# Kernel tuning notes

Hardware: AMD Instinct MI355X
Metric: run time of the kernel (lower is better)

The kernel has to match this reference:

```python
import jax, jax.numpy as jnp
import numpy as np

N_NODES = 100000
N_EDGES = 1600000
EMBED_DIM = 64
NUM_HEADS = 4
HEAD_DIM = EMBED_DIM // NUM_HEADS  # 16


def mish(x):
    return x * jnp.tanh(jax.nn.softplus(x))


def setup_inputs() -> dict:
    key = jax.random.key(0)
    ks = jax.random.split(key, 8)
    x = jax.random.normal(ks[0], (N_NODES, EMBED_DIM), dtype=jnp.float32)
    senders = jax.random.randint(ks[1], (N_EDGES,), 0, N_NODES, dtype=jnp.int32)
    receivers = jax.random.randint(ks[2], (N_EDGES,), 0, N_NODES, dtype=jnp.int32)
    sc = 1.0 / np.sqrt(EMBED_DIM)
    # DenseGeneral(features=(H, d)) for senders / receivers, with bias
    Ws = jax.random.normal(ks[3], (EMBED_DIM, NUM_HEADS, HEAD_DIM), dtype=jnp.float32) * sc
    bs = jnp.zeros((NUM_HEADS, HEAD_DIM), dtype=jnp.float32)
    Wr = jax.random.normal(ks[4], (EMBED_DIM, NUM_HEADS, HEAD_DIM), dtype=jnp.float32) * sc
    br = jnp.zeros((NUM_HEADS, HEAD_DIM), dtype=jnp.float32)
    # Dense(1) on last axis (head_dim), weights shared across heads
    aw = jax.random.normal(ks[5], (HEAD_DIM,), dtype=jnp.float32) * (1.0 / np.sqrt(HEAD_DIM))
    ab = jnp.zeros((1,), dtype=jnp.float32)
    return {"x": x, "Ws": Ws, "bs": bs, "Wr": Wr, "br": br,
            "aw": aw, "ab": ab, "senders": senders, "receivers": receivers}


def reference(x, Ws, bs, Wr, br, aw, ab, senders, receivers):
    n = x.shape[0]
    # Node-level projections (same math as per-edge DenseGeneral, less traffic)
    s_proj = jnp.einsum('nf,fhd->nhd', x, Ws) + bs  # [N,H,d]
    r_proj = jnp.einsum('nf,fhd->nhd', x, Wr) + br  # [N,H,d]
    se = s_proj[senders]      # [E,H,d] gather of sender features
    re = r_proj[receivers]    # [E,H,d] gather of receiver features
    # GATv2 logit: Dense(1)(mish(s + r)) -> [E,H]
    logits = jnp.einsum('ehd,d->eh', mish(se + re), aw) + ab[0]
    # Segment softmax over incoming edges of each receiver node
    lmax = jax.ops.segment_max(logits, receivers, num_segments=n)
    ex = jnp.exp(logits - lmax[receivers])
    denom = jax.ops.segment_sum(ex, receivers, num_segments=n)
    alpha = ex / denom[receivers]  # [E,H]
    # Scatter-sum weighted sender features back to receiver nodes
    out = jax.ops.segment_sum(alpha[..., None] * se, receivers, num_segments=n)  # [N,H,d]
    return out.reshape(n, -1)  # [N, H*d]
```

## Files before the change

### kernel.cpp

```cpp
#include <hip/hip_runtime.h>
#include <hip/hip_fp16.h>
#include <math.h>

#define N_NODES 100000
#define N_EDGES 1600000
#define EMBED 64
#define HEADS 4
#define HDIM 16

#define SLOTS 64

#define BKT_SHIFT 8
#define BKT_NODES 256
#define NBKT 391
#define BKT_CAP 5120
#define TILE 4096
#define NTILE 391
#define NGRP (N_EDGES / 4)

#define NODES_BLK 64
#define NBLK_PROJ 1563
#define SMEM_BYTES 52224

#define LOG2E 1.44269504f

__device__ __forceinline__ float mish_aw(float z, float awc) {
    float ex  = __expf(fminf(z, 30.f));
    float u   = 1.f + ex;
    float den = fmaf(u, u, 1.f);
    float f   = fmaf(-2.f, __builtin_amdgcn_rcpf(den), 1.f);
    return z * awc * f;
}

template<int CTRL>
__device__ __forceinline__ float ror_add(float t) {
    int x = __builtin_amdgcn_mov_dpp(__float_as_int(t), CTRL, 0xF, 0xF, true);
    return t + __int_as_float(x);
}
__device__ __forceinline__ float head_reduce(float t) {
    t = ror_add<0x121>(t);
    t = ror_add<0x122>(t);
    t = ror_add<0x124>(t);
    t = ror_add<0x128>(t);
    return t;
}

template<int CTRL>
__device__ __forceinline__ __half2 hror_add(__half2 t) {
    int x = __builtin_amdgcn_mov_dpp(__builtin_bit_cast(int, t), CTRL, 0xF, 0xF, true);
    return __hadd2(t, __builtin_bit_cast(__half2, x));
}
__device__ __forceinline__ __half2 head_reduce_h2(__half2 t) {
    t = hror_add<0x121>(t);
    t = hror_add<0x122>(t);
    t = hror_add<0x124>(t);
    t = hror_add<0x128>(t);
    return t;
}

__global__ __launch_bounds__(256) void proj_bucketa_kernel(
        const float* __restrict__ x,
        const float* __restrict__ Ws, const float* __restrict__ bs,
        const float* __restrict__ Wr, const float* __restrict__ br,
        const int* __restrict__ senders, const int* __restrict__ receivers,
        unsigned short* __restrict__ sph, unsigned short* __restrict__ rph,
        int* __restrict__ bktcnt, int* __restrict__ bkt) {
    __shared__ __align__(16) char smem[SMEM_BYTES];
    int tid = threadIdx.x;
    if (blockIdx.x < NBLK_PROJ) {
        float* wsT = (float*)smem;
        float* wrT = wsT + 64 * 68;
        float* xsh = wrT + 64 * 68;
        for (int i = tid; i < 4096; i += 256) {
            int k = i >> 6, o = i & 63;
            wsT[o * 68 + k] = Ws[i];
            wrT[o * 68 + k] = Wr[i];
        }
        int nb = blockIdx.x * NODES_BLK;
        for (int i = 0; i < 4; ++i) {
            int g = i * 256 + tid;
            int nl = g >> 4;
            int k4 = g & 15;
            if (nb + nl < N_NODES) {
                float4 v = ((const float4*)(x + ((size_t)(nb + nl) << 6)))[k4];
                *(float4*)(xsh + nl * 68 + (k4 << 2)) = v;
            }
        }
        __syncthreads();
        int o = tid & 63;
        int w = tid >> 6;
        float bsv = bs[o], brv = br[o];
        float accs[16], accr[16];
#pragma unroll
        for (int p = 0; p < 16; ++p) { accs[p] = bsv; accr[p] = brv; }
        const float4* ws4 = (const float4*)wsT + o * 17;
        const float4* wr4 = (const float4*)wrT + o * 17;
        const float4* xs4 = (const float4*)xsh + (w << 4) * 17;
#pragma unroll 4
        for (int k4 = 0; k4 < 16; ++k4) {
            float4 a = ws4[k4];
            float4 b = wr4[k4];
#pragma unroll
            for (int p = 0; p < 16; ++p) {
                float4 xv = xs4[p * 17 + k4];
                accs[p] += xv.x * a.x + xv.y * a.y + xv.z * a.z + xv.w * a.w;
                accr[p] += xv.x * b.x + xv.y * b.y + xv.z * b.z + xv.w * b.w;
            }
        }
        int node0 = nb + (w << 4);
#pragma unroll
        for (int p = 0; p < 16; ++p) {
            int node = node0 + p;
            if (node < N_NODES) {
                sph[(node << 6) + o] = __half_as_ushort(__float2half_rn(accs[p]));
                rph[(node << 6) + o] = __half_as_ushort(__float2half_rn(accr[p]));
            }
        }
    } else {
        int* hist = (int*)smem;
        int* base = hist + NBKT;
        int* cur  = base + NBKT;
        for (int i = tid; i < NBKT; i += 256) hist[i] = 0;
        __syncthreads();
        int g0 = (blockIdx.x - NBLK_PROJ) * (TILE / 4);
        int4 r[4], s[4];
        bool v[4];
#pragma unroll
        for (int t = 0; t < 4; ++t) {
            int g = g0 + t * 256 + tid;
            v[t] = (g < NGRP);
            if (v[t]) {
                r[t] = ((const int4*)receivers)[g];
                s[t] = ((const int4*)senders)[g];
                atomicAdd(&hist[r[t].x >> BKT_SHIFT], 1);
                atomicAdd(&hist[r[t].y >> BKT_SHIFT], 1);
                atomicAdd(&hist[r[t].z >> BKT_SHIFT], 1);
                atomicAdd(&hist[r[t].w >> BKT_SHIFT], 1);
            }
        }
        __syncthreads();
        for (int i = tid; i < NBKT; i += 256) {
            int h = hist[i];
            base[i] = (h > 0) ? atomicAdd(&bktcnt[i], h) : 0;
            cur[i] = 0;
        }
        __syncthreads();
#pragma unroll
        for (int t = 0; t < 4; ++t) {
            if (v[t]) {
                int b, rk, slot;
                b = r[t].x >> BKT_SHIFT; rk = atomicAdd(&cur[b], 1); slot = base[b] + rk;
                if (slot < BKT_CAP) bkt[b * BKT_CAP + slot] = ((r[t].x & (BKT_NODES - 1)) << 17) | s[t].x;
                b = r[t].y >> BKT_SHIFT; rk = atomicAdd(&cur[b], 1); slot = base[b] + rk;
                if (slot < BKT_CAP) bkt[b * BKT_CAP + slot] = ((r[t].y & (BKT_NODES - 1)) << 17) | s[t].y;
                b = r[t].z >> BKT_SHIFT; rk = atomicAdd(&cur[b], 1); slot = base[b] + rk;
                if (slot < BKT_CAP) bkt[b * BKT_CAP + slot] = ((r[t].z & (BKT_NODES - 1)) << 17) | s[t].z;
                b = r[t].w >> BKT_SHIFT; rk = atomicAdd(&cur[b], 1); slot = base[b] + rk;
                if (slot < BKT_CAP) bkt[b * BKT_CAP + slot] = ((r[t].w & (BKT_NODES - 1)) << 17) | s[t].w;
            }
        }
    }
}

__global__ __launch_bounds__(1024) void bucketb_kernel(
        const int* __restrict__ bktcnt, const int* __restrict__ bkt,
        int* __restrict__ cursor, int* __restrict__ csr) {
    __shared__ int lcur[BKT_NODES];
    int tid = threadIdx.x;
    int b = blockIdx.x;
    if (tid < BKT_NODES) lcur[tid] = 0;
    __syncthreads();
    int cnt = bktcnt[b];
    if (cnt > BKT_CAP) cnt = BKT_CAP;
    const int* bb = bkt + b * BKT_CAP;
    for (int i = tid; i < cnt; i += 1024) {
        int vv = bb[i];
        int rl = vv >> 17;
        int sv = vv & 0x1FFFF;
        int slot = atomicAdd(&lcur[rl], 1);
        if (slot < SLOTS) csr[((((b << BKT_SHIFT) + rl)) << 6) + slot] = sv << 7;
    }
    __syncthreads();
    if (tid < BKT_NODES) {
        int node = (b << BKT_SHIFT) + tid;
        if (node < N_NODES) cursor[node] = lcur[tid];
    }
}

__global__ __launch_bounds__(256) void fused_gather_kernel(
                                    const unsigned short* __restrict__ sph,
                                    const unsigned short* __restrict__ rph,
                                    const int* __restrict__ csr,
                                    const int* __restrict__ cursor,
                                    const float* __restrict__ aw,
                                    const float* __restrict__ ab,
                                    float* __restrict__ out) {
    int wave = (blockIdx.x * blockDim.x + threadIdx.x) >> 6;
    wave = __builtin_amdgcn_readfirstlane(wave);
    int lane = threadIdx.x & 63;
    int deg = cursor[wave];
    deg = (deg > SLOTS) ? SLOTS : deg;
    const int* cbase = csr + (wave << 6);
    const char* splb = (const char*)sph + (lane << 1);
    float rp  = __half2float(__ushort_as_half(rph[(wave << 6) + lane]));
    float awc = aw[lane & 15];
    __half2 k_pk   = __float2half2_rn(LOG2E);
    __half2 rpk_pk = __float2half2_rn(rp * LOG2E);
    __half2 aw2_pk = __float2half2_rn(awc * LOG2E);
    __half2 rpa_pk = __float2half2_rn(rp * awc * LOG2E);
    __half2 ones   = __float2half2_rn(1.0f);
    __half2 neg2   = __float2half2_rn(-2.0f);
    __half2 l2   = __float2half2_rn(0.0f);
    __half2 acc2 = __float2half2_rn(0.0f);
    float l_t = 0.f, acc_t = 0.f;
    int i = 0;
    for (; i + 8 <= deg; i += 8) {
        unsigned short su[8];
#pragma unroll
        for (int j = 0; j < 8; ++j) su[j] = *(const unsigned short*)(splb + cbase[i + j]);
#pragma unroll
        for (int j = 0; j < 4; ++j) {
            __half2 sp  = __halves2half2(__ushort_as_half(su[2 * j]),
                                         __ushort_as_half(su[2 * j + 1]));
            __half2 w   = h2exp2(__hfma2(sp, k_pk, rpk_pk));
            __half2 u   = __hadd2(w, ones);
            __half2 den = __hfma2(u, u, ones);
            __half2 r   = h2rcp(den);
            __half2 f   = __hfma2(neg2, r, ones);
            __half2 za  = __hfma2(sp, aw2_pk, rpa_pk);
            __half2 tt  = head_reduce_h2(__hmul2(za, f));
            __half2 p   = h2exp2(tt);
            l2   = __hadd2(l2, p);
            acc2 = __hfma2(p, sp, acc2);
        }
    }
    for (; i + 2 <= deg; i += 2) {
        __half2 sp  = __halves2half2(__ushort_as_half(*(const unsigned short*)(splb + cbase[i])),
                                     __ushort_as_half(*(const unsigned short*)(splb + cbase[i + 1])));
        __half2 w   = h2exp2(__hfma2(sp, k_pk, rpk_pk));
        __half2 u   = __hadd2(w, ones);
        __half2 den = __hfma2(u, u, ones);
        __half2 r   = h2rcp(den);
        __half2 f   = __hfma2(neg2, r, ones);
        __half2 za  = __hfma2(sp, aw2_pk, rpa_pk);
        __half2 tt  = head_reduce_h2(__hmul2(za, f));
        __half2 p   = h2exp2(tt);
        l2   = __hadd2(l2, p);
        acc2 = __hfma2(p, sp, acc2);
    }
    if (i < deg) {
        float sp0 = __half2float(__ushort_as_half(*(const unsigned short*)(splb + cbase[i])));
        float t0 = head_reduce(mish_aw(sp0 + rp, awc));
        float p = __builtin_amdgcn_exp2f(t0 * LOG2E);
        l_t += p;
        acc_t = fmaf(p, sp0, acc_t);
    }
    float l   = __low2float(l2) + __high2float(l2) + l_t;
    float acc = __low2float(acc2) + __high2float(acc2) + acc_t;
    out[(wave << 6) + lane] = (deg > 0) ? acc * __builtin_amdgcn_rcpf(l) : 0.f;
}

extern "C" void kernel_launch(void* const* d_in, const int* in_sizes, int n_in,
                              void* d_out, int out_size, void* d_ws, size_t ws_size,
                              hipStream_t stream) {
    const float* x  = (const float*)d_in[0];
    const float* Ws = (const float*)d_in[1];
    const float* bs = (const float*)d_in[2];
    const float* Wr = (const float*)d_in[3];
    const float* br = (const float*)d_in[4];
    const float* aw = (const float*)d_in[5];
    const float* ab = (const float*)d_in[6];
    const int* senders   = (const int*)d_in[7];
    const int* receivers = (const int*)d_in[8];
    float* out = (float*)d_out;

    char* wsp = (char*)d_ws;
    unsigned short* sph = (unsigned short*)wsp;  wsp += (size_t)N_NODES * EMBED * 2;
    unsigned short* rph = (unsigned short*)wsp;  wsp += (size_t)N_NODES * EMBED * 2;
    int* csr    = (int*)wsp;  wsp += (size_t)N_NODES * SLOTS * 4;
    int* cursor = (int*)wsp;  wsp += (size_t)N_NODES * 4;
    int* bkt    = (int*)wsp;  wsp += (size_t)NBKT * BKT_CAP * 4;
    int* bktcnt = (int*)wsp;  wsp += 512 * 4;

    hipMemsetAsync(bktcnt, 0, NBKT * 4, stream);

    proj_bucketa_kernel<<<NBLK_PROJ + NTILE, 256, 0, stream>>>(
        x, Ws, bs, Wr, br, senders, receivers, sph, rph, bktcnt, bkt);

    bucketb_kernel<<<NBKT, 1024, 0, stream>>>(bktcnt, bkt, cursor, csr);

    int gather_blocks = (N_NODES * 64 + 255) / 256;
    fused_gather_kernel<<<gather_blocks, 256, 0, stream>>>(sph, rph, csr, cursor,
                                                           aw, ab, out);
}
```

Baseline: 125.6 us.

## Reorder bucketing blocks first, halve tile size, prefetch gathers with split accumulators

After: 148.7 us. 1.18x slower.

```diff
diff --git a/kernel.cpp b/kernel.cpp
--- a/kernel.cpp
+++ b/kernel.cpp
@@ -14,8 +14,8 @@
 #define BKT_NODES 256
 #define NBKT 391
 #define BKT_CAP 5120
-#define TILE 4096
-#define NTILE 391
+#define TILE 2048
+#define NTILE 782
 #define NGRP (N_EDGES / 4)
 
 #define NODES_BLK 64
@@ -67,7 +67,7 @@
         int* __restrict__ bktcnt, int* __restrict__ bkt) {
     __shared__ __align__(16) char smem[SMEM_BYTES];
     int tid = threadIdx.x;
-    if (blockIdx.x < NBLK_PROJ) {
+    if (blockIdx.x >= NTILE) {
         float* wsT = (float*)smem;
         float* wrT = wsT + 64 * 68;
         float* xsh = wrT + 64 * 68;
@@ -76,7 +76,7 @@
             wsT[o * 68 + k] = Ws[i];
             wrT[o * 68 + k] = Wr[i];
         }
-        int nb = blockIdx.x * NODES_BLK;
+        int nb = (blockIdx.x - NTILE) * NODES_BLK;
         for (int i = 0; i < 4; ++i) {
             int g = i * 256 + tid;
             int nl = g >> 4;
@@ -122,11 +122,11 @@
         int* cur  = base + NBKT;
         for (int i = tid; i < NBKT; i += 256) hist[i] = 0;
         __syncthreads();
-        int g0 = (blockIdx.x - NBLK_PROJ) * (TILE / 4);
-        int4 r[4], s[4];
-        bool v[4];
-#pragma unroll
-        for (int t = 0; t < 4; ++t) {
+        int g0 = blockIdx.x * (TILE / 4);
+        int4 r[2], s[2];
+        bool v[2];
+#pragma unroll
+        for (int t = 0; t < 2; ++t) {
             int g = g0 + t * 256 + tid;
             v[t] = (g < NGRP);
             if (v[t]) {
@@ -146,7 +146,7 @@
         }
         __syncthreads();
 #pragma unroll
-        for (int t = 0; t < 4; ++t) {
+        for (int t = 0; t < 2; ++t) {
             if (v[t]) {
                 int b, rk, slot;
                 b = r[t].x >> BKT_SHIFT; rk = atomicAdd(&cur[b], 1); slot = base[b] + rk;
@@ -210,18 +210,25 @@
     __half2 rpa_pk = __float2half2_rn(rp * awc * LOG2E);
     __half2 ones   = __float2half2_rn(1.0f);
     __half2 neg2   = __float2half2_rn(-2.0f);
-    __half2 l2   = __float2half2_rn(0.0f);
-    __half2 acc2 = __float2half2_rn(0.0f);
+    __half2 l2a   = __float2half2_rn(0.0f), l2b   = __float2half2_rn(0.0f);
+    __half2 acc2a = __float2half2_rn(0.0f), acc2b = __float2half2_rn(0.0f);
     float l_t = 0.f, acc_t = 0.f;
-    int i = 0;
-    for (; i + 8 <= deg; i += 8) {
-        unsigned short su[8];
-#pragma unroll
-        for (int j = 0; j < 8; ++j) su[j] = *(const unsigned short*)(splb + cbase[i + j]);
+    int nb8 = deg >> 3;
+    unsigned short cur[8], nxt[8];
+    if (nb8 > 0) {
+#pragma unroll
+        for (int j = 0; j < 8; ++j) cur[j] = *(const unsigned short*)(splb + cbase[j]);
+    }
+    for (int k = 0; k < nb8; ++k) {
+        if (k + 1 < nb8) {
+            const int* cb = cbase + ((k + 1) << 3);
+#pragma unroll
+            for (int j = 0; j < 8; ++j) nxt[j] = *(const unsigned short*)(splb + cb[j]);
+        }
 #pragma unroll
         for (int j = 0; j < 4; ++j) {
-            __half2 sp  = __halves2half2(__ushort_as_half(su[2 * j]),
-                                         __ushort_as_half(su[2 * j + 1]));
+            __half2 sp  = __halves2half2(__ushort_as_half(cur[2 * j]),
+                                         __ushort_as_half(cur[2 * j + 1]));
             __half2 w   = h2exp2(__hfma2(sp, k_pk, rpk_pk));
             __half2 u   = __hadd2(w, ones);
             __half2 den = __hfma2(u, u, ones);
@@ -230,10 +237,13 @@
             __half2 za  = __hfma2(sp, aw2_pk, rpa_pk);
             __half2 tt  = head_reduce_h2(__hmul2(za, f));
             __half2 p   = h2exp2(tt);
-            l2   = __hadd2(l2, p);
-            acc2 = __hfma2(p, sp, acc2);
-        }
-    }
+            if (j & 1) { l2b = __hadd2(l2b, p); acc2b = __hfma2(p, sp, acc2b); }
+            else       { l2a = __hadd2(l2a, p); acc2a = __hfma2(p, sp, acc2a); }
+        }
+#pragma unroll
+        for (int j = 0; j < 8; ++j) cur[j] = nxt[j];
+    }
+    int i = nb8 << 3;
     for (; i + 2 <= deg; i += 2) {
         __half2 sp  = __halves2half2(__ushort_as_half(*(const unsigned short*)(splb + cbase[i])),
                                      __ushort_as_half(*(const unsigned short*)(splb + cbase[i + 1])));
@@ -245,8 +255,8 @@
         __half2 za  = __hfma2(sp, aw2_pk, rpa_pk);
         __half2 tt  = head_reduce_h2(__hmul2(za, f));
         __half2 p   = h2exp2(tt);
-        l2   = __hadd2(l2, p);
-        acc2 = __hfma2(p, sp, acc2);
+        l2a   = __hadd2(l2a, p);
+        acc2a = __hfma2(p, sp, acc2a);
     }
     if (i < deg) {
         float sp0 = __half2float(__ushort_as_half(*(const unsigned short*)(splb + cbase[i])));
@@ -255,6 +265,8 @@
         l_t += p;
         acc_t = fmaf(p, sp0, acc_t);
     }
+    __half2 l2   = __hadd2(l2a, l2b);
+    __half2 acc2 = __hadd2(acc2a, acc2b);
     float l   = __low2float(l2) + __high2float(l2) + l_t;
     float acc = __low2float(acc2) + __high2float(acc2) + acc_t;
     out[(wave << 6) + lane] = (deg > 0) ? acc * __builtin_amdgcn_rcpf(l) : 0.f;
@@ -284,7 +296,7 @@
 
     hipMemsetAsync(bktcnt, 0, NBKT * 4, stream);
 
-    proj_bucketa_kernel<<<NBLK_PROJ + NTILE, 256, 0, stream>>>(
+    proj_bucketa_kernel<<<NTILE + NBLK_PROJ, 256, 0, stream>>>(
         x, Ws, bs, Wr, br, senders, receivers, sph, rph, bktcnt, bkt);
 
     bucketb_kernel<<<NBKT, 1024, 0, stream>>>(bktcnt, bkt, cursor, csr);
```

## Double-buffer sender gathers and mask tail batch in edge softmax loop

Applied to the files above, without the earlier changes.

After: 134.2 us. +6.8%, slower.

```diff
diff --git a/kernel.cpp b/kernel.cpp
--- a/kernel.cpp
+++ b/kernel.cpp
@@ -23,27 +23,6 @@
 #define SMEM_BYTES 52224
 
 #define LOG2E 1.44269504f
-
-__device__ __forceinline__ float mish_aw(float z, float awc) {
-    float ex  = __expf(fminf(z, 30.f));
-    float u   = 1.f + ex;
-    float den = fmaf(u, u, 1.f);
-    float f   = fmaf(-2.f, __builtin_amdgcn_rcpf(den), 1.f);
-    return z * awc * f;
-}
-
-template<int CTRL>
-__device__ __forceinline__ float ror_add(float t) {
-    int x = __builtin_amdgcn_mov_dpp(__float_as_int(t), CTRL, 0xF, 0xF, true);
-    return t + __int_as_float(x);
-}
-__device__ __forceinline__ float head_reduce(float t) {
-    t = ror_add<0x121>(t);
-    t = ror_add<0x122>(t);
-    t = ror_add<0x124>(t);
-    t = ror_add<0x128>(t);
-    return t;
-}
 
 template<int CTRL>
 __device__ __forceinline__ __half2 hror_add(__half2 t) {
@@ -210,54 +189,74 @@
     __half2 rpa_pk = __float2half2_rn(rp * awc * LOG2E);
     __half2 ones   = __float2half2_rn(1.0f);
     __half2 neg2   = __float2half2_rn(-2.0f);
-    __half2 l2   = __float2half2_rn(0.0f);
-    __half2 acc2 = __float2half2_rn(0.0f);
-    float l_t = 0.f, acc_t = 0.f;
-    int i = 0;
-    for (; i + 8 <= deg; i += 8) {
-        unsigned short su[8];
-#pragma unroll
-        for (int j = 0; j < 8; ++j) su[j] = *(const unsigned short*)(splb + cbase[i + j]);
-#pragma unroll
-        for (int j = 0; j < 4; ++j) {
-            __half2 sp  = __halves2half2(__ushort_as_half(su[2 * j]),
-                                         __ushort_as_half(su[2 * j + 1]));
-            __half2 w   = h2exp2(__hfma2(sp, k_pk, rpk_pk));
-            __half2 u   = __hadd2(w, ones);
-            __half2 den = __hfma2(u, u, ones);
-            __half2 r   = h2rcp(den);
-            __half2 f   = __hfma2(neg2, r, ones);
-            __half2 za  = __hfma2(sp, aw2_pk, rpa_pk);
-            __half2 tt  = head_reduce_h2(__hmul2(za, f));
-            __half2 p   = h2exp2(tt);
-            l2   = __hadd2(l2, p);
-            acc2 = __hfma2(p, sp, acc2);
-        }
-    }
-    for (; i + 2 <= deg; i += 2) {
-        __half2 sp  = __halves2half2(__ushort_as_half(*(const unsigned short*)(splb + cbase[i])),
-                                     __ushort_as_half(*(const unsigned short*)(splb + cbase[i + 1])));
-        __half2 w   = h2exp2(__hfma2(sp, k_pk, rpk_pk));
-        __half2 u   = __hadd2(w, ones);
-        __half2 den = __hfma2(u, u, ones);
-        __half2 r   = h2rcp(den);
-        __half2 f   = __hfma2(neg2, r, ones);
-        __half2 za  = __hfma2(sp, aw2_pk, rpa_pk);
-        __half2 tt  = head_reduce_h2(__hmul2(za, f));
-        __half2 p   = h2exp2(tt);
-        l2   = __hadd2(l2, p);
-        acc2 = __hfma2(p, sp, acc2);
-    }
-    if (i < deg) {
-        float sp0 = __half2float(__ushort_as_half(*(const unsigned short*)(splb + cbase[i])));
-        float t0 = head_reduce(mish_aw(sp0 + rp, awc));
-        float p = __builtin_amdgcn_exp2f(t0 * LOG2E);
-        l_t += p;
-        acc_t = fmaf(p, sp0, acc_t);
-    }
-    float l   = __low2float(l2) + __high2float(l2) + l_t;
-    float acc = __low2float(acc2) + __high2float(acc2) + acc_t;
-    out[(wave << 6) + lane] = (deg > 0) ? acc * __builtin_amdgcn_rcpf(l) : 0.f;
+    __half2 l2a   = __float2half2_rn(0.0f), l2b   = __float2half2_rn(0.0f);
+    __half2 acc2a = __float2half2_rn(0.0f), acc2b = __float2half2_rn(0.0f);
+
+    float res = 0.f;
+    if (deg > 0) {
+        int nbt = (deg + 7) >> 3;
+        int off0 = cbase[0];
+        unsigned short bufA[8], bufB[8];
+
+#define LOADB(dst, m)                                                          \
+        {                                                                      \
+            int i0m = (m) << 3;                                                \
+            bool lastm = ((m) == nbt - 1);                                     \
+            _Pragma("unroll")                                                  \
+            for (int j = 0; j < 8; ++j) {                                      \
+                int idx = i0m + j;                                             \
+                int off = cbase[idx];               \
+                if (lastm) off = (idx < deg) ? off : off0;     \
+                dst[j] = *(const unsigned short*)(splb + off);                 \
+            }                                                                  \
+        }
+
+#define COMPUTE(buf, kk)                                                       \
+        {                                                                      \
+            bool last = ((kk) == nbt - 1);                                     \
+            int i0c = (kk) << 3;                                               \
+            _Pragma("unroll")                                                  \
+            for (int j = 0; j < 4; ++j) {                                      \
+                __half2 sp  = __halves2half2(__ushort_as_half(buf[2 * j]),     \
+                                             __ushort_as_half(buf[2 * j + 1]));\
+                __half2 w   = h2exp2(__hfma2(sp, k_pk, rpk_pk));               \
+                __half2 u   = __hadd2(w, ones);                                \
+                __half2 den = __hfma2(u, u, ones);                             \
+                __half2 r   = h2rcp(den);                                      \
+                __half2 f   = __hfma2(neg2, r, ones);                          \
+                __half2 za  = __hfma2(sp, aw2_pk, rpa_pk);                     \
+                __half2 tt  = head_reduce_h2(__hmul2(za, f));                  \
+                __half2 p   = h2exp2(tt);                                      \
+                if (last) {                                                    \
+                    unsigned m = ((i0c + 2 * j)     < deg ? 0x0000FFFFu : 0u)  \
+                               | ((i0c + 2 * j + 1) < deg ? 0xFFFF0000u : 0u); \
+                    p = __builtin_bit_cast(__half2,                            \
+                            (unsigned)(__builtin_bit_cast(unsigned, p) & m));  \
+                }                                                              \
+                if (j & 1) { l2b = __hadd2(l2b, p); acc2b = __hfma2(p, sp, acc2b); } \
+                else       { l2a = __hadd2(l2a, p); acc2a = __hfma2(p, sp, acc2a); } \
+            }                                                                  \
+        }
+
+        LOADB(bufA, 0);
+        int k = 0;
+        while (true) {
+            if (k + 1 < nbt) LOADB(bufB, k + 1);
+            COMPUTE(bufA, k);
+            ++k; if (k >= nbt) break;
+            if (k + 1 < nbt) LOADB(bufA, k + 1);
+            COMPUTE(bufB, k);
+            ++k; if (k >= nbt) break;
+        }
+#undef LOADB
+#undef COMPUTE
+        __half2 l2   = __hadd2(l2a, l2b);
+        __half2 acc2 = __hadd2(acc2a, acc2b);
+        float l   = __low2float(l2) + __high2float(l2);
+        float acc = __low2float(acc2) + __high2float(acc2);
+        res = acc * __builtin_amdgcn_rcpf(l);
+    }
+    out[(wave << 6) + lane] = res;
 }
 
 extern "C" void kernel_launch(void* const* d_in, const int* in_sizes, int n_in,
```
